# Kernel tuning notes

Measured on AMD Instinct MI355X. Metric: run time of the kernel, lower is better.

Reference implementation:

```python
import jax, jax.numpy as jnp
from jax import lax
import numpy as np

LAM = 0.2
MAX_ITER = 10
EPS = 1e-07
WIN_SIZE = 2
COS_EPS = 1e-5
L, B, D = 1024, 32, 256


def setup_inputs() -> dict:
    key = jax.random.key(0)
    k1, k2, k3 = jax.random.split(key, 3)
    m1 = jax.random.normal(k1, (L, B, D), dtype=jnp.float32)
    m2 = jax.random.normal(k2, (L, B, D), dtype=jnp.float32)
    lengths = jax.random.randint(k3, (B,), L // 2, L + 1, dtype=jnp.int32)
    return {"m1": m1, "m2": m2, "lengths": lengths}


def _sinkhorn_item(x, y, l):
    # x, y: (L, D) padded; l: scalar valid length
    Lm = x.shape[0]
    idx = jnp.arange(Lm)
    mask = idx < l                              # (L,) valid rows/cols
    mm = mask[:, None] & mask[None, :]          # (L, L) valid block

    # cosine distance: 1 - cos_sim with eps clamp (matches nn.CosineSimilarity)
    xn = x / jnp.maximum(jnp.linalg.norm(x, axis=-1, keepdims=True), COS_EPS)
    yn = y / jnp.maximum(jnp.linalg.norm(y, axis=-1, keepdims=True), COS_EPS)
    M = 1.0 - xn @ yn.T                          # (L, L)
    # band penalty: +100 outside |i-j| <= win_size
    band = jnp.abs(idx[:, None] - idx[None, :]) > WIN_SIZE
    M = M + 100.0 * band

    lf = l.astype(M.dtype)
    r = jnp.where(mask, 1.0 / lf, 0.0)           # row marginals 1/n on valid prefix
    c = r                                        # col marginals (n == m == l)

    P = jnp.exp(-LAM * M) * mm
    P = P / jnp.sum(P)
    u0 = jnp.zeros(Lm, dtype=M.dtype)

    def step(carry, _):
        P, u, active = carry
        usum = jnp.sum(P, axis=1)
        cond = active & (jnp.max(jnp.abs(u - usum)) > EPS)
        u_new = usum
        scale_r = jnp.where(mask, r / jnp.where(mask, u_new, 1.0), 0.0)
        P1 = P * scale_r[:, None]
        s = jnp.sum(P1, axis=0)
        # NOTE: original torch code reshapes (c / P.sum(0)) to (-1, 1), i.e.
        # applies the column-sum correction along ROWS (works since n == m).
        # We reproduce that exactly for faithfulness.
        scale_c = jnp.where(mask, c / jnp.where(mask, s, 1.0), 0.0)
        P2 = P1 * scale_c[:, None]
        P_out = jnp.where(cond, P2, P)
        u_out = jnp.where(cond, u_new, u)
        return (P_out, u_out, cond), None

    (P, _, _), _ = lax.scan(step, (P, u0, jnp.array(True)), None, length=MAX_ITER)

    # final: P / P.sum(-1)  -- torch broadcasting divides column j by rowsum[j]
    rowsum = jnp.sum(P, axis=-1)
    rs = jnp.where(mask, rowsum, 1.0)
    P_norm = jnp.where(mm, P / rs[None, :], 0.0)
    cost = jnp.sum(P * M)
    return P_norm, cost


def _forward(m1, m2, lengths):
    # m1, m2: (L, B, D) -> vmap over batch axis 1
    f = jax.vmap(_sinkhorn_item, in_axes=(1, 1, 0))
    P, cost = f(m1, m2, lengths)                 # (B, L, L), (B,)
    return P, cost


def reference(m1, m2, lengths):
    return _forward(m1, m2, lengths)
```

## Files before the change

kernel.cpp:

```cpp
#include <hip/hip_runtime.h>
#include <math.h>

#define L 1024
#define NB 32
#define DD 256
#define LAM_F 0.2f
#define EPS_F 1e-7f

__device__ __forceinline__ float wave_reduce_sum(float v) {
#pragma unroll
    for (int m = 1; m < 64; m <<= 1) v += __shfl_xor(v, m, 64);
    return v;
}

__global__ void __launch_bounds__(256) norms_dots_kernel(
        const float* __restrict__ m1, const float* __restrict__ m2,
        float* __restrict__ dots, float* __restrict__ xn2o, float* __restrict__ yn2o) {
    const int wave = threadIdx.x >> 6, lane = threadIdx.x & 63;
    const int blk = blockIdx.x;
    const int b = blk >> 8;
    const int i = ((blk & 255) << 2) | wave;
    const float4 xv = ((const float4*)(m1 + (size_t)(i * NB + b) * DD))[lane];
    float xn2 = xv.x * xv.x + xv.y * xv.y + xv.z * xv.z + xv.w * xv.w;
    float yn2 = 0.f;
    float dt[5];
#pragma unroll
    for (int o = 0; o < 5; ++o) {
        int j = i + o - 2;
        float d = 0.f;
        if (j >= 0 && j < L) {
            const float4 yv = ((const float4*)(m2 + (size_t)(j * NB + b) * DD))[lane];
            d = xv.x * yv.x + xv.y * yv.y + xv.z * yv.z + xv.w * yv.w;
            if (o == 2) yn2 = yv.x * yv.x + yv.y * yv.y + yv.z * yv.z + yv.w * yv.w;
        }
        dt[o] = d;
    }
    xn2 = wave_reduce_sum(xn2);
    yn2 = wave_reduce_sum(yn2);
#pragma unroll
    for (int o = 0; o < 5; ++o) dt[o] = wave_reduce_sum(dt[o]);
    if (lane == 0) {
        const int r = b * L + i;
        xn2o[r] = xn2;
        yn2o[r] = yn2;
#pragma unroll
        for (int o = 0; o < 5; ++o) dots[r * 5 + o] = dt[o];
    }
}

__global__ void __launch_bounds__(1024) sinkhorn_kernel(
        const float* __restrict__ dots, const float* __restrict__ xn2,
        const float* __restrict__ yn2, const int* __restrict__ lengths,
        float* __restrict__ oband, float* __restrict__ cost_out) {
    __shared__ float Pb[L * 5];
    __shared__ float Mb[L * 5];
    __shared__ float inv_ny[L];
    __shared__ float u[L];
    __shared__ float rs[L];
    __shared__ float red[16];

    const int b = blockIdx.x;
    const int i = threadIdx.x;
    const int wv = i >> 6, ln = i & 63;
    const int l = lengths[b];
    const float rmarg = 1.0f / (float)l;
    const int base = b * L + i;

    const float inv_nx = 1.0f / fmaxf(sqrtf(xn2[base]), 1e-5f);
    inv_ny[i] = 1.0f / fmaxf(sqrtf(yn2[base]), 1e-5f);
    u[i] = 0.f;
    __syncthreads();

    float psum = 0.f;
#pragma unroll
    for (int o = 0; o < 5; ++o) {
        int j = i + o - 2;
        float M = 0.f, P = 0.f;
        if (j >= 0 && j < L && i < l && j < l) {
            M = 1.0f - dots[base * 5 + o] * inv_nx * inv_ny[j];
            P = expf(-LAM_F * M);
        }
        Mb[i * 5 + o] = M;
        Pb[i * 5 + o] = P;
        psum += P;
    }
    psum = wave_reduce_sum(psum);
    if (ln == 0) red[wv] = psum;
    __syncthreads();
    float total = 0.f;
#pragma unroll
    for (int k = 0; k < 16; ++k) total += red[k];
    __syncthreads();
    const float inv_total = 1.0f / total;
#pragma unroll
    for (int o = 0; o < 5; ++o) Pb[i * 5 + o] *= inv_total;

    for (int it = 0; it < 10; ++it) {
        float us = Pb[i * 5 + 0] + Pb[i * 5 + 1] + Pb[i * 5 + 2] + Pb[i * 5 + 3] + Pb[i * 5 + 4];
        float diff = fabsf(u[i] - us);
#pragma unroll
        for (int m = 1; m < 64; m <<= 1) diff = fmaxf(diff, __shfl_xor(diff, m, 64));
        if (ln == 0) red[wv] = diff;
        __syncthreads();
        float maxdiff = red[0];
#pragma unroll
        for (int k = 1; k < 16; ++k) maxdiff = fmaxf(maxdiff, red[k]);
        __syncthreads();
        if (maxdiff <= EPS_F) break;

        u[i] = us;
        const float sr = (i < l) ? rmarg / us : 0.f;
#pragma unroll
        for (int o = 0; o < 5; ++o) Pb[i * 5 + o] *= sr;
        __syncthreads();

        float s = 0.f;
#pragma unroll
        for (int d = -2; d <= 2; ++d) {
            int rr = i + d;
            if (rr >= 0 && rr < L) s += Pb[rr * 5 + (2 - d)];
        }
        __syncthreads();
        const float sc = (i < l) ? rmarg / s : 0.f;
#pragma unroll
        for (int o = 0; o < 5; ++o) Pb[i * 5 + o] *= sc;
        __syncthreads();
    }

    const float rsum = Pb[i * 5 + 0] + Pb[i * 5 + 1] + Pb[i * 5 + 2] + Pb[i * 5 + 3] + Pb[i * 5 + 4];
    rs[i] = (i < l) ? rsum : 1.0f;
    float cp = 0.f;
#pragma unroll
    for (int o = 0; o < 5; ++o) cp += Pb[i * 5 + o] * Mb[i * 5 + o];
    cp = wave_reduce_sum(cp);
    if (ln == 0) red[wv] = cp;
    __syncthreads();
    if (i == 0) {
        float cost = 0.f;
#pragma unroll
        for (int k = 0; k < 16; ++k) cost += red[k];
        cost_out[b] = cost;
    }
#pragma unroll
    for (int o = 0; o < 5; ++o) {
        int j = i + o - 2;
        int jc = min(max(j, 0), L - 1);
        oband[base * 5 + o] = Pb[i * 5 + o] / rs[jc];
    }
}

__global__ void __launch_bounds__(256) write_kernel(
        const float* __restrict__ oband, float* __restrict__ out) {
    const int t = blockIdx.x * 256 + threadIdx.x;
    const int b = t >> 18;
    const int rem = t & 262143;
    const int i = rem >> 8;
    const int j0 = (rem & 255) << 2;
    float4 v = make_float4(0.f, 0.f, 0.f, 0.f);
    if (j0 + 3 >= i - 2 && j0 <= i + 2) {
        const float* ob = oband + (size_t)((b << 10) + i) * 5;
        float vv[4];
#pragma unroll
        for (int k = 0; k < 4; ++k) {
            int o = j0 + k - i;
            vv[k] = (o >= -2 && o <= 2) ? ob[o + 2] : 0.f;
        }
        v = make_float4(vv[0], vv[1], vv[2], vv[3]);
    }
    ((float4*)out)[t] = v;
}

extern "C" void kernel_launch(void* const* d_in, const int* in_sizes, int n_in,
                              void* d_out, int out_size, void* d_ws, size_t ws_size,
                              hipStream_t stream) {
    const float* m1 = (const float*)d_in[0];
    const float* m2 = (const float*)d_in[1];
    const int* lengths = (const int*)d_in[2];
    float* out = (float*)d_out;
    float* ws = (float*)d_ws;

    float* dots  = ws;
    float* xn2   = dots + NB * L * 5;
    float* yn2   = xn2 + NB * L;
    float* oband = yn2 + NB * L;

    norms_dots_kernel<<<NB * (L / 4), 256, 0, stream>>>(m1, m2, dots, xn2, yn2);
    sinkhorn_kernel<<<NB, L, 0, stream>>>(dots, xn2, yn2, lengths, oband,
                                          out + (size_t)NB * L * L);
    write_kernel<<<(NB * L * L / 4) / 256, 256, 0, stream>>>(oband, out);
}
```

Measured before the change: 198.3 us.

## Fuse zero-fill into prep kernel and run Sinkhorn in one wave with registers

The prep kernel now stages the m2 rows into LDS so each is read once per 16-row tile. The same launch also zero-fills the full output matrix, which removes the separate write kernel and the oband intermediate. Sinkhorn runs as a single 64-lane wave per batch item: each lane owns 16 rows in registers, and P is kept as its initial value times an accumulated per-row scale, so block barriers become wave shuffles. The band values are then scattered straight into the output, at the cost of heavy register use, only 32 waves total, and a write ordering that relies on the fill kernel finishing first.

```diff
diff --git a/kernel.cpp b/kernel.cpp
--- a/kernel.cpp
+++ b/kernel.cpp
@@ -7,38 +7,63 @@
 #define LAM_F 0.2f
 #define EPS_F 1e-7f
 
-__device__ __forceinline__ float wave_reduce_sum(float v) {
+#define NDBLK (NB * (L / 16))
+#define FILLBLK (NB * L * L / 4 / 1024)
+
+__device__ __forceinline__ float wave_sum(float v) {
 #pragma unroll
     for (int m = 1; m < 64; m <<= 1) v += __shfl_xor(v, m, 64);
     return v;
 }
-
-__global__ void __launch_bounds__(256) norms_dots_kernel(
+__device__ __forceinline__ float wave_max(float v) {
+#pragma unroll
+    for (int m = 1; m < 64; m <<= 1) v = fmaxf(v, __shfl_xor(v, m, 64));
+    return v;
+}
+__device__ __forceinline__ float dot4(float4 a, float4 b) {
+    return a.x * b.x + a.y * b.y + a.z * b.z + a.w * b.w;
+}
+
+__global__ void __launch_bounds__(1024) prep_kernel(
         const float* __restrict__ m1, const float* __restrict__ m2,
-        float* __restrict__ dots, float* __restrict__ xn2o, float* __restrict__ yn2o) {
-    const int wave = threadIdx.x >> 6, lane = threadIdx.x & 63;
-    const int blk = blockIdx.x;
-    const int b = blk >> 8;
-    const int i = ((blk & 255) << 2) | wave;
+        float* __restrict__ dots, float* __restrict__ xn2o, float* __restrict__ yn2o,
+        float* __restrict__ out) {
+    if (blockIdx.x >= NDBLK) {
+        size_t t = (size_t)(blockIdx.x - NDBLK) * 1024 + threadIdx.x;
+        ((float4*)out)[t] = make_float4(0.f, 0.f, 0.f, 0.f);
+        return;
+    }
+    __shared__ float ysh[20 * DD];
+    const int b = blockIdx.x >> 6;
+    const int i0 = (blockIdx.x & 63) << 4;
+    for (int f = threadIdx.x; f < 20 * (DD / 4); f += 1024) {
+        int srow = f >> 6, l4 = f & 63;
+        int j = i0 - 2 + srow;
+        if (j >= 0 && j < L)
+            ((float4*)ysh)[f] = ((const float4*)(m2 + (size_t)(j * NB + b) * DD))[l4];
+    }
+    __syncthreads();
+    const int w = threadIdx.x >> 6, lane = threadIdx.x & 63;
+    const int i = i0 + w;
     const float4 xv = ((const float4*)(m1 + (size_t)(i * NB + b) * DD))[lane];
-    float xn2 = xv.x * xv.x + xv.y * xv.y + xv.z * xv.z + xv.w * xv.w;
-    float yn2 = 0.f;
+    float xn2 = dot4(xv, xv);
+    const float4 yself = ((const float4*)(ysh + (w + 2) * DD))[lane];
+    float yn2 = dot4(yself, yself);
     float dt[5];
 #pragma unroll
     for (int o = 0; o < 5; ++o) {
         int j = i + o - 2;
         float d = 0.f;
         if (j >= 0 && j < L) {
-            const float4 yv = ((const float4*)(m2 + (size_t)(j * NB + b) * DD))[lane];
-            d = xv.x * yv.x + xv.y * yv.y + xv.z * yv.z + xv.w * yv.w;
-            if (o == 2) yn2 = yv.x * yv.x + yv.y * yv.y + yv.z * yv.z + yv.w * yv.w;
+            const float4 y2 = ((const float4*)(ysh + (w + o) * DD))[lane];
+            d = dot4(xv, y2);
         }
         dt[o] = d;
     }
-    xn2 = wave_reduce_sum(xn2);
-    yn2 = wave_reduce_sum(yn2);
-#pragma unroll
-    for (int o = 0; o < 5; ++o) dt[o] = wave_reduce_sum(dt[o]);
+    xn2 = wave_sum(xn2);
+    yn2 = wave_sum(yn2);
+#pragma unroll
+    for (int o = 0; o < 5; ++o) dt[o] = wave_sum(dt[o]);
     if (lane == 0) {
         const int r = b * L + i;
         xn2o[r] = xn2;
@@ -48,126 +73,151 @@
     }
 }
 
-__global__ void __launch_bounds__(1024) sinkhorn_kernel(
+__global__ void __launch_bounds__(64) sinkhorn_kernel(
         const float* __restrict__ dots, const float* __restrict__ xn2,
         const float* __restrict__ yn2, const int* __restrict__ lengths,
-        float* __restrict__ oband, float* __restrict__ cost_out) {
-    __shared__ float Pb[L * 5];
-    __shared__ float Mb[L * 5];
-    __shared__ float inv_ny[L];
-    __shared__ float u[L];
-    __shared__ float rs[L];
-    __shared__ float red[16];
-
+        float* __restrict__ out) {
     const int b = blockIdx.x;
-    const int i = threadIdx.x;
-    const int wv = i >> 6, ln = i & 63;
+    const int lane = threadIdx.x;
     const int l = lengths[b];
     const float rmarg = 1.0f / (float)l;
-    const int base = b * L + i;
-
-    const float inv_nx = 1.0f / fmaxf(sqrtf(xn2[base]), 1e-5f);
-    inv_ny[i] = 1.0f / fmaxf(sqrtf(yn2[base]), 1e-5f);
-    u[i] = 0.f;
-    __syncthreads();
-
-    float psum = 0.f;
-#pragma unroll
-    for (int o = 0; o < 5; ++o) {
-        int j = i + o - 2;
-        float M = 0.f, P = 0.f;
-        if (j >= 0 && j < L && i < l && j < l) {
-            M = 1.0f - dots[base * 5 + o] * inv_nx * inv_ny[j];
-            P = expf(-LAM_F * M);
-        }
-        Mb[i * 5 + o] = M;
-        Pb[i * 5 + o] = P;
-        psum += P;
-    }
-    psum = wave_reduce_sum(psum);
-    if (ln == 0) red[wv] = psum;
-    __syncthreads();
-    float total = 0.f;
-#pragma unroll
-    for (int k = 0; k < 16; ++k) total += red[k];
-    __syncthreads();
-    const float inv_total = 1.0f / total;
-#pragma unroll
-    for (int o = 0; o < 5; ++o) Pb[i * 5 + o] *= inv_total;
+    const int r0 = lane << 4;
+
+    float inv_nx[16], inv_ny[16];
+#pragma unroll
+    for (int k = 0; k < 16; ++k) {
+        const int base = b * L + r0 + k;
+        inv_nx[k] = 1.0f / fmaxf(sqrtf(xn2[base]), 1e-5f);
+        inv_ny[k] = 1.0f / fmaxf(sqrtf(yn2[base]), 1e-5f);
+    }
+    float nyext[20];
+    nyext[0] = __shfl_up(inv_ny[14], 1, 64);
+    nyext[1] = __shfl_up(inv_ny[15], 1, 64);
+#pragma unroll
+    for (int k = 0; k < 16; ++k) nyext[k + 2] = inv_ny[k];
+    nyext[18] = __shfl_down(inv_ny[0], 1, 64);
+    nyext[19] = __shfl_down(inv_ny[1], 1, 64);
+
+    float P0[16][5], p0sum[16], pm0[16];
+#pragma unroll
+    for (int k = 0; k < 16; ++k) {
+        const int i = r0 + k;
+        const int base = b * L + i;
+        p0sum[k] = 0.f;
+        pm0[k] = 0.f;
+#pragma unroll
+        for (int o = 0; o < 5; ++o) {
+            const int j = i + o - 2;
+            const float dv = dots[base * 5 + o];
+            const float M = 1.0f - dv * inv_nx[k] * nyext[k + o];
+            const bool valid = (j >= 0) && (j < L) && (i < l) && (j < l);
+            const float P = valid ? expf(-LAM_F * M) : 0.0f;
+            P0[k][o] = P;
+            p0sum[k] += P;
+            pm0[k] += P * M;
+        }
+    }
+    float tot = 0.f;
+#pragma unroll
+    for (int k = 0; k < 16; ++k) tot += p0sum[k];
+    tot = wave_sum(tot);
+    const float inv_total = 1.0f / tot;
+    float sacc[16], u[16];
+#pragma unroll
+    for (int k = 0; k < 16; ++k) { sacc[k] = inv_total; u[k] = 0.f; }
+
+    const float pA = __shfl_up(P0[14][4], 1, 64);
+    const float pB = __shfl_up(P0[15][3], 1, 64);
+    const float pC = __shfl_up(P0[15][4], 1, 64);
+    const float pE = __shfl_down(P0[0][0], 1, 64);
+    const float pD = __shfl_down(P0[0][1], 1, 64);
+    const float pF = __shfl_down(P0[1][0], 1, 64);
 
     for (int it = 0; it < 10; ++it) {
-        float us = Pb[i * 5 + 0] + Pb[i * 5 + 1] + Pb[i * 5 + 2] + Pb[i * 5 + 3] + Pb[i * 5 + 4];
-        float diff = fabsf(u[i] - us);
-#pragma unroll
-        for (int m = 1; m < 64; m <<= 1) diff = fmaxf(diff, __shfl_xor(diff, m, 64));
-        if (ln == 0) red[wv] = diff;
-        __syncthreads();
-        float maxdiff = red[0];
-#pragma unroll
-        for (int k = 1; k < 16; ++k) maxdiff = fmaxf(maxdiff, red[k]);
-        __syncthreads();
-        if (maxdiff <= EPS_F) break;
-
-        u[i] = us;
-        const float sr = (i < l) ? rmarg / us : 0.f;
-#pragma unroll
-        for (int o = 0; o < 5; ++o) Pb[i * 5 + o] *= sr;
-        __syncthreads();
-
-        float s = 0.f;
-#pragma unroll
-        for (int d = -2; d <= 2; ++d) {
-            int rr = i + d;
-            if (rr >= 0 && rr < L) s += Pb[rr * 5 + (2 - d)];
-        }
-        __syncthreads();
-        const float sc = (i < l) ? rmarg / s : 0.f;
-#pragma unroll
-        for (int o = 0; o < 5; ++o) Pb[i * 5 + o] *= sc;
-        __syncthreads();
-    }
-
-    const float rsum = Pb[i * 5 + 0] + Pb[i * 5 + 1] + Pb[i * 5 + 2] + Pb[i * 5 + 3] + Pb[i * 5 + 4];
-    rs[i] = (i < l) ? rsum : 1.0f;
-    float cp = 0.f;
-#pragma unroll
-    for (int o = 0; o < 5; ++o) cp += Pb[i * 5 + o] * Mb[i * 5 + o];
-    cp = wave_reduce_sum(cp);
-    if (ln == 0) red[wv] = cp;
-    __syncthreads();
-    if (i == 0) {
-        float cost = 0.f;
-#pragma unroll
-        for (int k = 0; k < 16; ++k) cost += red[k];
-        cost_out[b] = cost;
-    }
-#pragma unroll
-    for (int o = 0; o < 5; ++o) {
-        int j = i + o - 2;
-        int jc = min(max(j, 0), L - 1);
-        oband[base * 5 + o] = Pb[i * 5 + o] / rs[jc];
-    }
-}
-
-__global__ void __launch_bounds__(256) write_kernel(
-        const float* __restrict__ oband, float* __restrict__ out) {
-    const int t = blockIdx.x * 256 + threadIdx.x;
-    const int b = t >> 18;
-    const int rem = t & 262143;
-    const int i = rem >> 8;
-    const int j0 = (rem & 255) << 2;
-    float4 v = make_float4(0.f, 0.f, 0.f, 0.f);
-    if (j0 + 3 >= i - 2 && j0 <= i + 2) {
-        const float* ob = oband + (size_t)((b << 10) + i) * 5;
-        float vv[4];
-#pragma unroll
-        for (int k = 0; k < 4; ++k) {
-            int o = j0 + k - i;
-            vv[k] = (o >= -2 && o <= 2) ? ob[o + 2] : 0.f;
-        }
-        v = make_float4(vv[0], vv[1], vv[2], vv[3]);
-    }
-    ((float4*)out)[t] = v;
+        float us[16], diff = 0.f;
+#pragma unroll
+        for (int k = 0; k < 16; ++k) {
+            us[k] = p0sum[k] * sacc[k];
+            diff = fmaxf(diff, fabsf(u[k] - us[k]));
+        }
+        diff = wave_max(diff);
+        if (diff <= EPS_F) break;
+
+        float s1[16];
+#pragma unroll
+        for (int k = 0; k < 16; ++k) {
+            u[k] = us[k];
+            const float sr = (r0 + k < l) ? rmarg / us[k] : 0.0f;
+            s1[k] = sacc[k] * sr;
+        }
+        float s1ext[20];
+        {
+            float a = __shfl_up(s1[14], 1, 64), c = __shfl_up(s1[15], 1, 64);
+            float d = __shfl_down(s1[0], 1, 64), e = __shfl_down(s1[1], 1, 64);
+            s1ext[0] = (lane == 0) ? 0.f : a;
+            s1ext[1] = (lane == 0) ? 0.f : c;
+            s1ext[18] = (lane == 63) ? 0.f : d;
+            s1ext[19] = (lane == 63) ? 0.f : e;
+        }
+#pragma unroll
+        for (int k = 0; k < 16; ++k) s1ext[k + 2] = s1[k];
+
+        float s[16];
+#pragma unroll
+        for (int k = 0; k < 16; ++k) {
+            float acc = P0[k][2] * s1ext[k + 2];
+            acc += ((k >= 2) ? P0[k - 2][4] : ((k == 0) ? pA : pC)) * s1ext[k];
+            acc += ((k >= 1) ? P0[k - 1][3] : pB) * s1ext[k + 1];
+            acc += ((k <= 14) ? P0[k + 1][1] : pD) * s1ext[k + 3];
+            acc += ((k <= 13) ? P0[k + 2][0] : ((k == 14) ? pE : pF)) * s1ext[k + 4];
+            s[k] = acc;
+        }
+#pragma unroll
+        for (int k = 0; k < 16; ++k) {
+            const float sc = (r0 + k < l) ? rmarg / s[k] : 0.0f;
+            sacc[k] = s1[k] * sc;
+        }
+    }
+
+    float rs[16];
+#pragma unroll
+    for (int k = 0; k < 16; ++k) rs[k] = (r0 + k < l) ? p0sum[k] * sacc[k] : 1.0f;
+    float rsext[20];
+    rsext[0] = __shfl_up(rs[14], 1, 64);
+    rsext[1] = __shfl_up(rs[15], 1, 64);
+#pragma unroll
+    for (int k = 0; k < 16; ++k) rsext[k + 2] = rs[k];
+    rsext[18] = __shfl_down(rs[0], 1, 64);
+    rsext[19] = __shfl_down(rs[1], 1, 64);
+
+    float cpart = 0.f;
+#pragma unroll
+    for (int k = 0; k < 16; ++k) cpart += pm0[k] * sacc[k];
+    cpart = wave_sum(cpart);
+    if (lane == 0) out[(size_t)NB * L * L + b] = cpart;
+
+#pragma unroll
+    for (int k = 0; k < 16; ++k) {
+        const int i = r0 + k;
+        const float pv0 = P0[k][0] * sacc[k] / rsext[k + 0];
+        const float pv1 = P0[k][1] * sacc[k] / rsext[k + 1];
+        const float pv2 = P0[k][2] * sacc[k] / rsext[k + 2];
+        const float pv3 = P0[k][3] * sacc[k] / rsext[k + 3];
+        const float pv4 = P0[k][4] * sacc[k] / rsext[k + 4];
+        const int c0 = (i - 2 > 0 ? i - 2 : 0) >> 2;
+        const int c1 = (i + 2 < L - 1 ? i + 2 : L - 1) >> 2;
+        float4* orow = (float4*)(out + ((size_t)b * L + i) * L);
+        for (int c = c0; c <= c1; ++c) {
+            float e[4];
+#pragma unroll
+            for (int t = 0; t < 4; ++t) {
+                const int o = 4 * c + t - i + 2;
+                e[t] = (o == 0) ? pv0 : (o == 1) ? pv1 : (o == 2) ? pv2
+                       : (o == 3) ? pv3 : (o == 4) ? pv4 : 0.0f;
+            }
+            orow[c] = make_float4(e[0], e[1], e[2], e[3]);
+        }
+    }
 }
 
 extern "C" void kernel_launch(void* const* d_in, const int* in_sizes, int n_in,
@@ -179,13 +229,10 @@
     float* out = (float*)d_out;
     float* ws = (float*)d_ws;
 
-    float* dots  = ws;
-    float* xn2   = dots + NB * L * 5;
-    float* yn2   = xn2 + NB * L;
-    float* oband = yn2 + NB * L;
-
-    norms_dots_kernel<<<NB * (L / 4), 256, 0, stream>>>(m1, m2, dots, xn2, yn2);
-    sinkhorn_kernel<<<NB, L, 0, stream>>>(dots, xn2, yn2, lengths, oband,
-                                          out + (size_t)NB * L * L);
-    write_kernel<<<(NB * L * L / 4) / 256, 256, 0, stream>>>(oband, out);
-}
+    float* dots = ws;
+    float* xn2 = dots + NB * L * 5;
+    float* yn2 = xn2 + NB * L;
+
+    prep_kernel<<<NDBLK + FILLBLK, 1024, 0, stream>>>(m1, m2, dots, xn2, yn2, out);
+    sinkhorn_kernel<<<NB, 64, 0, stream>>>(dots, xn2, yn2, lengths, out);
+}
```

New measurement: 200.2 us. About the same (+0.9%).
